# Kernel tuning notes

Hardware: AMD Instinct MI355X
Metric: run time of the kernel (lower is better)

The kernel has to match this reference:

```python
import jax, jax.numpy as jnp
import numpy as np

B, S, H, NH = 1, 2048, 1024, 16
HD = H // NH
LAYER_NUMBER = 1
EPS = 1e-5
NEG_INF = -1e9


def _layernorm(x, g, b):
    mu = jnp.mean(x, axis=-1, keepdims=True)
    var = jnp.mean((x - mu) ** 2, axis=-1, keepdims=True)
    return (x - mu) * jax.lax.rsqrt(var + EPS) * g + b


def _bloom_gelu(x):
    # tanh approximation used by Megatron/Bloom
    return x * 0.5 * (1.0 + jnp.tanh(0.79788456 * x * (1.0 + 0.044715 * x * x)))


def setup_inputs() -> dict:
    key = jax.random.key(0)
    ks = jax.random.split(key, 8)

    def w(k, shape, scale=0.02):
        return jax.random.normal(k, shape, jnp.float32) * scale

    # additive causal mask: 0 where attended, -1e9 where masked
    causal = jnp.where(jnp.tril(jnp.ones((S, S), bool)), 0.0, NEG_INF).astype(jnp.float32)
    attention_mask = causal[None, None]  # [1,1,S,S]

    return {
        "hidden_states": jax.random.normal(ks[0], (B, S, H), jnp.float32),
        "attention_mask": attention_mask,
        "alibi": w(ks[1], (B * NH, 1, S), 1.0),
        "ln1_g": jnp.ones((H,), jnp.float32),
        "ln1_b": jnp.zeros((H,), jnp.float32),
        "qkv_w": w(ks[2], (3 * H, H)),
        "qkv_b": jnp.zeros((3 * H,), jnp.float32),
        "dense_w": w(ks[3], (H, H)),
        "dense_b": jnp.zeros((H,), jnp.float32),
        "ln2_g": jnp.ones((H,), jnp.float32),
        "ln2_b": jnp.zeros((H,), jnp.float32),
        "fc1_w": w(ks[4], (4 * H, H)),
        "fc1_b": jnp.zeros((4 * H,), jnp.float32),
        "fc2_w": w(ks[5], (H, 4 * H)),
        "fc2_b": jnp.zeros((H,), jnp.float32),
    }


def reference(hidden_states, attention_mask, alibi,
              ln1_g, ln1_b, qkv_w, qkv_b, dense_w, dense_b,
              ln2_g, ln2_b, fc1_w, fc1_b, fc2_w, fc2_b):
    dtype = hidden_states.dtype
    norm_factor = np.sqrt(HD).astype(np.float32) * LAYER_NUMBER
    beta = 1.0 / LAYER_NUMBER

    # --- input layernorm (residual = pre-LN hidden states) ---
    ln_out = _layernorm(hidden_states, ln1_g, ln1_b)
    residual = hidden_states

    # --- attention ---
    fused = ln_out @ qkv_w.T + qkv_b                      # [B,S,3H]
    fused = fused.reshape(B, S, NH, 3 * HD)
    q, k, v = fused[..., :HD], fused[..., HD:2 * HD], fused[..., 2 * HD:]

    scores = jnp.einsum('bqhd,bkhd->bhqk', q, k) / norm_factor \
             + beta * alibi.reshape(B, NH, 1, S)          # [B,NH,S,S]
    attn = scores * LAYER_NUMBER + attention_mask
    attn = jnp.maximum(attn, jnp.finfo(attn.dtype).min)
    probs = jax.nn.softmax(attn.astype(jnp.float32), axis=-1).astype(dtype)
    probs = probs * (attention_mask == 0.0)               # zero out masked positions

    ctx = jnp.einsum('bhqk,bkhd->bqhd', probs, v).reshape(B, S, H)
    attn_out = ctx @ dense_w.T + dense_b + residual       # dropout_add, p=0

    # --- post-attention layernorm + MLP ---
    ln2_out = _layernorm(attn_out, ln2_g, ln2_b)
    residual2 = attn_out
    h = _bloom_gelu(ln2_out @ fc1_w.T + fc1_b)            # [B,S,4H]
    out = h @ fc2_w.T + fc2_b + residual2                 # dropout_add, p=0
    return out
```

## Files before the change

### kernel.cpp

```cpp
#include <hip/hip_runtime.h>
#include <hip/hip_bf16.h>

typedef unsigned short u16;
typedef __attribute__((ext_vector_type(8))) short bf16x8;
typedef __attribute__((ext_vector_type(4))) float f32x4;

typedef __attribute__((address_space(1))) const void cgvoid;
typedef __attribute__((address_space(3))) void lvoid;

static __device__ __forceinline__ u16 f2bf(float x) {
    __hip_bfloat16 h = __float2bfloat16(x);
    return __builtin_bit_cast(u16, h);
}

static __device__ __forceinline__ void gload_lds16(const u16* g, u16* l) {
    __builtin_amdgcn_global_load_lds((cgvoid*)g, (lvoid*)l, 16, 0, 0);
}

__global__ __launch_bounds__(256) void cvt_f32_bf16(
    const float* __restrict__ in, u16* __restrict__ out, int n4)
{
    int i = blockIdx.x * blockDim.x + threadIdx.x;
    const int stride = gridDim.x * blockDim.x;
    for (; i < n4; i += stride) {
        const float4 v = ((const float4*)in)[i];
        ushort4 pk;
        pk.x = f2bf(v.x); pk.y = f2bf(v.y); pk.z = f2bf(v.z); pk.w = f2bf(v.w);
        ((ushort4*)out)[i] = pk;
    }
}

__global__ __launch_bounds__(256) void ln_bf16(
    const float* __restrict__ x, const float* __restrict__ gw,
    const float* __restrict__ bw, u16* __restrict__ out)
{
    const int row = blockIdx.x;
    const int t = threadIdx.x;
    const float4 v = ((const float4*)(x + (size_t)row * 1024))[t];
    float s  = v.x + v.y + v.z + v.w;
    float sq = v.x*v.x + v.y*v.y + v.z*v.z + v.w*v.w;
#pragma unroll
    for (int d = 1; d < 64; d <<= 1) {
        s  += __shfl_xor(s, d, 64);
        sq += __shfl_xor(sq, d, 64);
    }
    __shared__ float ss[4], ssq[4];
    const int wave = t >> 6, lane = t & 63;
    if (lane == 0) { ss[wave] = s; ssq[wave] = sq; }
    __syncthreads();
    s  = ss[0] + ss[1] + ss[2] + ss[3];
    sq = ssq[0] + ssq[1] + ssq[2] + ssq[3];
    const float mu = s * (1.f / 1024.f);
    const float rinv = rsqrtf(sq * (1.f / 1024.f) - mu * mu + 1e-5f);
    const float4 gv = ((const float4*)gw)[t];
    const float4 bv = ((const float4*)bw)[t];
    ushort4 pk;
    pk.x = f2bf((v.x - mu) * rinv * gv.x + bv.x);
    pk.y = f2bf((v.y - mu) * rinv * gv.y + bv.y);
    pk.z = f2bf((v.z - mu) * rinv * gv.z + bv.z);
    pk.w = f2bf((v.w - mu) * rinv * gv.w + bv.w);
    ((ushort4*)(out + (size_t)row * 1024))[t] = pk;
}

template<int EPI, int BN>
__global__ __launch_bounds__(256, 4) void gemm_bt(
    const u16* __restrict__ A, const u16* __restrict__ Bw,
    const float* __restrict__ bias, void* __restrict__ Cout,
    float* __restrict__ p0, float* __restrict__ pext,
    int M, int N, int K, int Kspan)
{
    constexpr int WC = BN / 64;
    constexpr int MI = (BN == 128) ? 4 : 2;
    constexpr int NI = 4;
    __shared__ __align__(16) u16 As[128 * 64];
    __shared__ __align__(16) u16 Bs[BN * 64];
    const int t = threadIdx.x;
    const int lane = t & 63;
    const int wave = t >> 6;
    const int wr = wave / WC, wc = wave % WC;
    const int g = lane >> 4, r16 = lane & 15;
    const int tile_m = blockIdx.x * 128;
    const int tile_n = blockIdx.y * BN;
    const int kb = blockIdx.z * Kspan;

    f32x4 acc[MI][NI] = {};

    for (int k0 = kb; k0 < kb + Kspan; k0 += 64) {
        __syncthreads();
#pragma unroll
        for (int i = 0; i < 4; ++i) {
            const int off = (t + i * 256) * 8;
            const int row = off >> 6;
            const int col = off & 63;
            gload_lds16(A + (size_t)(tile_m + row) * K + k0 + col, As + off);
        }
#pragma unroll
        for (int i = 0; i < BN / 32; ++i) {
            const int off = (t + i * 256) * 8;
            const int row = off >> 6;
            const int col = off & 63;
            gload_lds16(Bw + (size_t)(tile_n + row) * K + k0 + col, Bs + off);
        }
        __syncthreads();

        bf16x8 af[MI][2], bfr[NI][2];
#pragma unroll
        for (int mi = 0; mi < MI; ++mi)
#pragma unroll
            for (int ks = 0; ks < 2; ++ks)
                af[mi][ks] = *(const bf16x8*)(As + (wr*(MI*16) + mi*16 + r16)*64 + ks*32 + g*8);
#pragma unroll
        for (int ni = 0; ni < NI; ++ni)
#pragma unroll
            for (int ks = 0; ks < 2; ++ks)
                bfr[ni][ks] = *(const bf16x8*)(Bs + (wc*64 + ni*16 + r16)*64 + ks*32 + g*8);
#pragma unroll
        for (int mi = 0; mi < MI; ++mi)
#pragma unroll
            for (int ni = 0; ni < NI; ++ni) {
                acc[mi][ni] = __builtin_amdgcn_mfma_f32_16x16x32_bf16(af[mi][0], bfr[ni][0], acc[mi][ni], 0, 0, 0);
                acc[mi][ni] = __builtin_amdgcn_mfma_f32_16x16x32_bf16(af[mi][1], bfr[ni][1], acc[mi][ni], 0, 0, 0);
            }
    }

    float* dst = nullptr;
    if constexpr (EPI == 4)
        dst = (blockIdx.z == 0) ? p0 : pext + (size_t)(blockIdx.z - 1) * ((size_t)M * N);

#pragma unroll
    for (int mi = 0; mi < MI; ++mi) {
#pragma unroll
        for (int ni = 0; ni < NI; ++ni) {
            const int col = tile_n + wc*64 + ni*16 + r16;
            const int row0 = tile_m + wr*(MI*16) + mi*16 + g*4;
#pragma unroll
            for (int r = 0; r < 4; ++r) {
                const int row = row0 + r;
                if constexpr (EPI == 4) {
                    dst[(size_t)row * N + col] = acc[mi][ni][r];
                } else if constexpr (EPI == 0) {
                    ((u16*)Cout)[(size_t)row * N + col] = f2bf(acc[mi][ni][r] + bias[col]);
                } else {
                    const float v = acc[mi][ni][r] + bias[col];
                    const float c = 0.79788456f * v * (1.0f + 0.044715f * v * v);
                    ((u16*)Cout)[(size_t)row * N + col] = f2bf(v / (1.0f + __expf(-2.0f * c)));
                }
            }
        }
    }
}

template<int NP>
__global__ __launch_bounds__(256) void reduce_bias_res(
    const float* __restrict__ p0, const float* __restrict__ pext,
    const float* __restrict__ bias, const float* __restrict__ res,
    float* __restrict__ out, int n4, int n4row)
{
    int i = blockIdx.x * blockDim.x + threadIdx.x;
    const int stride = gridDim.x * blockDim.x;
    for (; i < n4; i += stride) {
        float4 a = ((const float4*)p0)[i];
#pragma unroll
        for (int j = 0; j < NP - 1; ++j) {
            const float4 b = ((const float4*)pext)[(size_t)j * n4 + i];
            a.x += b.x; a.y += b.y; a.z += b.z; a.w += b.w;
        }
        const float4 bv = ((const float4*)bias)[i & (n4row - 1)];
        const float4 rv = ((const float4*)res)[i];
        float4 o;
        o.x = a.x + bv.x + rv.x;
        o.y = a.y + bv.y + rv.y;
        o.z = a.z + bv.z + rv.z;
        o.w = a.w + bv.w + rv.w;
        ((float4*)out)[i] = o;
    }
}

__global__ __launch_bounds__(256) void pack_kv(
    const u16* __restrict__ fused, u16* __restrict__ kP, u16* __restrict__ vP)
{
    const int bid = blockIdx.x;
    const int h = bid >> 5, kt = bid & 31;
    const int kt0 = kt * 64;
    const int t = threadIdx.x;
    const int lane = t & 63;
    const int g = lane >> 4, r16 = lane & 15;
    const size_t tbase = ((size_t)(h * 32 + kt)) * 4096;

#pragma unroll
    for (int half = 0; half < 2; ++half) {
        const int gi = (t >> 6) + half * 4;
        const int kn = gi >> 1, ks = gi & 1;
        const int w = 32*(kn>>1) + 8*(r16>>2) + 4*(kn&1) + (r16&3);
        const bf16x8 kv = *(const bf16x8*)(fused + (size_t)(kt0 + w) * 3072 + h*192 + 64 + ks*32 + g*8);
        *(bf16x8*)(kP + tbase + gi*512 + lane*8) = kv;
        union { bf16x8 v; u16 e[8]; } uv;
        const u16* vs = fused + (size_t)(kt0 + ks*32 + g*8) * 3072 + h*192 + 128 + kn*16 + r16;
#pragma unroll
        for (int e = 0; e < 8; ++e) uv.e[e] = vs[(size_t)e * 3072];
        *(bf16x8*)(vP + tbase + gi*512 + lane*8) = uv.v;
    }
}

__global__ __launch_bounds__(256, 4) void attn_swapped(
    const u16* __restrict__ fused, const u16* __restrict__ kP,
    const u16* __restrict__ vP, const float* __restrict__ alibi,
    u16* __restrict__ ctx)
{
    const int bid = blockIdx.x;
    const int h = bid & 15;
    const int qt = 127 - (bid >> 4);
    const int qw0 = qt * 16;
    const int t = threadIdx.x;
    const int lane = t & 63, wave = t >> 6;
    const int g = lane >> 4, r16 = lane & 15;
    const int qrow = qw0 + r16;

    __shared__ float Ms[4][16], Ls[4][16];
    __shared__ float Os[4][4][16][17];

    const u16* qbase = fused + (size_t)qrow * 3072 + h * 192;
    bf16x8 qf[2];
    qf[0] = *(const bf16x8*)(qbase + g*8);
    qf[1] = *(const bf16x8*)(qbase + 32 + g*8);

    f32x4 o_acc[4] = {};
    float m_r = -3.0e38f, l_r = 0.f;

    const u16* kPh = kP + (size_t)h * 32 * 4096;
    const u16* vPh = vP + (size_t)h * 32 * 4096;
    const float* abase = alibi + (size_t)h * 2048;

    const int nkt = (qw0 >> 6) + 1;
    for (int kt = wave; kt < nkt; kt += 4) {
        const int kt0 = kt * 64;
        const u16* kT = kPh + (size_t)kt * 4096;
        const u16* vT = vPh + (size_t)kt * 4096;

        bf16x8 kf[4][2], vf[4][2];
#pragma unroll
        for (int kn = 0; kn < 4; ++kn) {
            kf[kn][0] = *(const bf16x8*)(kT + (kn*2 + 0)*512 + lane*8);
            kf[kn][1] = *(const bf16x8*)(kT + (kn*2 + 1)*512 + lane*8);
        }
        float4 al[4];
#pragma unroll
        for (int kn = 0; kn < 4; ++kn)
            al[kn] = *(const float4*)(abase + kt0 + 32*(kn>>1) + 8*g + 4*(kn&1));
#pragma unroll
        for (int nd = 0; nd < 4; ++nd) {
            vf[nd][0] = *(const bf16x8*)(vT + (nd*2 + 0)*512 + lane*8);
            vf[nd][1] = *(const bf16x8*)(vT + (nd*2 + 1)*512 + lane*8);
        }

        f32x4 sc[4] = {};
#pragma unroll
        for (int kn = 0; kn < 4; ++kn) {
            sc[kn] = __builtin_amdgcn_mfma_f32_16x16x32_bf16(kf[kn][0], qf[0], sc[kn], 0, 0, 0);
            sc[kn] = __builtin_amdgcn_mfma_f32_16x16x32_bf16(kf[kn][1], qf[1], sc[kn], 0, 0, 0);
        }

        float s[4][4];
        float rmax = -3.0e38f;
#pragma unroll
        for (int kn = 0; kn < 4; ++kn) {
            const int kb = kt0 + 32*(kn>>1) + 8*g + 4*(kn&1);
            const float alv[4] = {al[kn].x, al[kn].y, al[kn].z, al[kn].w};
#pragma unroll
            for (int r = 0; r < 4; ++r) {
                float v = sc[kn][r] * 0.125f + alv[r];
                v = (kb + r <= qrow) ? v : -1.0e30f;
                s[kn][r] = v;
                rmax = fmaxf(rmax, v);
            }
        }
        rmax = fmaxf(rmax, __shfl_xor(rmax, 16, 64));
        rmax = fmaxf(rmax, __shfl_xor(rmax, 32, 64));

        const float mnew = fmaxf(m_r, rmax);
        const float scale = __expf(m_r - mnew);
        m_r = mnew;

        float psum = 0.f;
        u16 ph[4][4];
#pragma unroll
        for (int kn = 0; kn < 4; ++kn)
#pragma unroll
            for (int r = 0; r < 4; ++r) {
                const float p = __expf(s[kn][r] - mnew);
                psum += p;
                ph[kn][r] = f2bf(p);
            }
        psum += __shfl_xor(psum, 16, 64);
        psum += __shfl_xor(psum, 32, 64);
        l_r = l_r * scale + psum;

#pragma unroll
        for (int nd = 0; nd < 4; ++nd)
#pragma unroll
            for (int r = 0; r < 4; ++r)
                o_acc[nd][r] *= scale;

        bf16x8 pf[2];
#pragma unroll
        for (int ks = 0; ks < 2; ++ks) {
            union { bf16x8 v; u16 e[8]; } u;
#pragma unroll
            for (int r = 0; r < 4; ++r) { u.e[r] = ph[2*ks][r]; u.e[4+r] = ph[2*ks+1][r]; }
            pf[ks] = u.v;
        }
#pragma unroll
        for (int nd = 0; nd < 4; ++nd) {
            o_acc[nd] = __builtin_amdgcn_mfma_f32_16x16x32_bf16(vf[nd][0], pf[0], o_acc[nd], 0, 0, 0);
            o_acc[nd] = __builtin_amdgcn_mfma_f32_16x16x32_bf16(vf[nd][1], pf[1], o_acc[nd], 0, 0, 0);
        }
    }

#pragma unroll
    for (int nd = 0; nd < 4; ++nd)
#pragma unroll
        for (int r = 0; r < 4; ++r)
            Os[wave][nd][g*4 + r][r16] = o_acc[nd][r];
    if (g == 0) { Ms[wave][r16] = m_r; Ls[wave][r16] = l_r; }
    __syncthreads();

    if (wave == 0) {
        const float m0 = Ms[0][r16], m1 = Ms[1][r16], m2 = Ms[2][r16], m3 = Ms[3][r16];
        const float ms = fmaxf(fmaxf(m0, m1), fmaxf(m2, m3));
        const float f0 = __expf(m0 - ms), f1 = __expf(m1 - ms);
        const float f2 = __expf(m2 - ms), f3 = __expf(m3 - ms);
        const float l = f0*Ls[0][r16] + f1*Ls[1][r16] + f2*Ls[2][r16] + f3*Ls[3][r16];
        const float inv = 1.0f / l;
#pragma unroll
        for (int nd = 0; nd < 4; ++nd) {
            float v[4];
#pragma unroll
            for (int r = 0; r < 4; ++r) {
                const int d = g*4 + r;
                v[r] = (f0*Os[0][nd][d][r16] + f1*Os[1][nd][d][r16] +
                        f2*Os[2][nd][d][r16] + f3*Os[3][nd][d][r16]) * inv;
            }
            ushort4 pk;
            pk.x = f2bf(v[0]); pk.y = f2bf(v[1]); pk.z = f2bf(v[2]); pk.w = f2bf(v[3]);
            *(ushort4*)(ctx + (size_t)qrow * 1024 + h*64 + nd*16 + g*4) = pk;
        }
    }
}

extern "C" void kernel_launch(void* const* d_in, const int* in_sizes, int n_in,
                              void* d_out, int out_size, void* d_ws, size_t ws_size,
                              hipStream_t stream)
{
    (void)in_sizes; (void)n_in; (void)out_size; (void)ws_size;
    const float* hidden  = (const float*)d_in[0];
    const float* alibi   = (const float*)d_in[2];
    const float* ln1_g   = (const float*)d_in[3];
    const float* ln1_b   = (const float*)d_in[4];
    const float* qkv_w   = (const float*)d_in[5];
    const float* qkv_b   = (const float*)d_in[6];
    const float* dense_w = (const float*)d_in[7];
    const float* dense_b = (const float*)d_in[8];
    const float* ln2_g   = (const float*)d_in[9];
    const float* ln2_b   = (const float*)d_in[10];
    const float* fc1_w   = (const float*)d_in[11];
    const float* fc1_b   = (const float*)d_in[12];
    const float* fc2_w   = (const float*)d_in[13];
    const float* fc2_b   = (const float*)d_in[14];
    float* out = (float*)d_out;

    char* p = (char*)d_ws;
    u16* ln_buf   = (u16*)p;  p += (size_t)2048 * 1024 * 2;
    u16* qkv_wb   = (u16*)p;  p += (size_t)3072 * 1024 * 2;
    u16* fusedq   = (u16*)p;  p += (size_t)2048 * 3072 * 2;
    u16* ctx      = (u16*)p;  p += (size_t)2048 * 1024 * 2;
    u16* dense_wb = (u16*)p;  p += (size_t)1024 * 1024 * 2;
    float* attn_o = (float*)p; p += (size_t)2048 * 1024 * 4;
    u16* fc1_wb   = (u16*)p;  p += (size_t)4096 * 1024 * 2;
    u16* fc2_wb   = (u16*)p;  p += (size_t)1024 * 4096 * 2;
    float* pext   = (float*)p; p += (size_t)3 * 2048 * 1024 * 4;
    u16* hbuf = fusedq;
    u16* kP = (u16*)attn_o;
    u16* vP = kP + (size_t)16 * 32 * 4096;
    float* part0 = (float*)d_ws;

    cvt_f32_bf16<<<2048, 256, 0, stream>>>(qkv_w,   qkv_wb,   3072*1024/4);
    cvt_f32_bf16<<<1024, 256, 0, stream>>>(dense_w, dense_wb, 1024*1024/4);
    cvt_f32_bf16<<<2048, 256, 0, stream>>>(fc1_w,   fc1_wb,   4096*1024/4);
    cvt_f32_bf16<<<2048, 256, 0, stream>>>(fc2_w,   fc2_wb,   1024*4096/4);

    ln_bf16<<<2048, 256, 0, stream>>>(hidden, ln1_g, ln1_b, ln_buf);
    gemm_bt<0,64><<<dim3(16, 48), 256, 0, stream>>>(ln_buf, qkv_wb, qkv_b, fusedq,
                                                    nullptr, nullptr, 2048, 3072, 1024, 1024);
    pack_kv<<<512, 256, 0, stream>>>(fusedq, kP, vP);
    attn_swapped<<<2048, 256, 0, stream>>>(fusedq, kP, vP, alibi, ctx);
    gemm_bt<4,64><<<dim3(16, 16, 2), 256, 0, stream>>>(ctx, dense_wb, nullptr, nullptr,
                                                       part0, pext, 2048, 1024, 1024, 512);
    reduce_bias_res<2><<<2048, 256, 0, stream>>>(part0, pext, dense_b, hidden, attn_o,
                                                 2048*1024/4, 256);
    ln_bf16<<<2048, 256, 0, stream>>>(attn_o, ln2_g, ln2_b, ln_buf);
    gemm_bt<2,64><<<dim3(16, 64), 256, 0, stream>>>(ln_buf, fc1_wb, fc1_b, hbuf,
                                                    nullptr, nullptr, 2048, 4096, 1024, 1024);
    gemm_bt<4,64><<<dim3(16, 16, 4), 256, 0, stream>>>(hbuf, fc2_wb, nullptr, nullptr,
                                                       part0, pext, 2048, 1024, 4096, 1024);
    reduce_bias_res<4><<<2048, 256, 0, stream>>>(part0, pext, fc2_b, attn_o, out,
                                                 2048*1024/4, 256);
}
```

Baseline: 177.7 us.

## Fuse weight conversions with LN1 and split-K reduce with LN2

```diff
diff --git a/kernel.cpp b/kernel.cpp
--- a/kernel.cpp
+++ b/kernel.cpp
@@ -17,49 +17,60 @@
     __builtin_amdgcn_global_load_lds((cgvoid*)g, (lvoid*)l, 16, 0, 0);
 }
 
-__global__ __launch_bounds__(256) void cvt_f32_bf16(
-    const float* __restrict__ in, u16* __restrict__ out, int n4)
-{
-    int i = blockIdx.x * blockDim.x + threadIdx.x;
-    const int stride = gridDim.x * blockDim.x;
-    for (; i < n4; i += stride) {
-        const float4 v = ((const float4*)in)[i];
+__global__ __launch_bounds__(256) void prep(
+    const float* __restrict__ hidden, const float* __restrict__ g1,
+    const float* __restrict__ b1, u16* __restrict__ ln_out,
+    const float* __restrict__ qkv_w, const float* __restrict__ dense_w,
+    const float* __restrict__ fc1_w, const float* __restrict__ fc2_w,
+    u16* __restrict__ qkv_wb, u16* __restrict__ dense_wb,
+    u16* __restrict__ fc1_wb, u16* __restrict__ fc2_wb)
+{
+    const int t = threadIdx.x;
+    if (blockIdx.x < 2048) {
+        const int row = blockIdx.x;
+        const float4 v = ((const float4*)(hidden + (size_t)row * 1024))[t];
+        float s  = v.x + v.y + v.z + v.w;
+        float sq = v.x*v.x + v.y*v.y + v.z*v.z + v.w*v.w;
+#pragma unroll
+        for (int d = 1; d < 64; d <<= 1) {
+            s  += __shfl_xor(s, d, 64);
+            sq += __shfl_xor(sq, d, 64);
+        }
+        __shared__ float ss[4], ssq[4];
+        const int wave = t >> 6, lane = t & 63;
+        if (lane == 0) { ss[wave] = s; ssq[wave] = sq; }
+        __syncthreads();
+        s  = ss[0] + ss[1] + ss[2] + ss[3];
+        sq = ssq[0] + ssq[1] + ssq[2] + ssq[3];
+        const float mu = s * (1.f / 1024.f);
+        const float rinv = rsqrtf(sq * (1.f / 1024.f) - mu * mu + 1e-5f);
+        const float4 gv = ((const float4*)g1)[t];
+        const float4 bv = ((const float4*)b1)[t];
+        ushort4 pk;
+        pk.x = f2bf((v.x - mu) * rinv * gv.x + bv.x);
+        pk.y = f2bf((v.y - mu) * rinv * gv.y + bv.y);
+        pk.z = f2bf((v.z - mu) * rinv * gv.z + bv.z);
+        pk.w = f2bf((v.w - mu) * rinv * gv.w + bv.w);
+        ((ushort4*)(ln_out + (size_t)row * 1024))[t] = pk;
+        return;
+    }
+    constexpr int C0 = 786432;
+    constexpr int C1 = C0 + 262144;
+    constexpr int C2 = C1 + 1048576;
+    constexpr int C3 = C2 + 1048576;
+    int i = (blockIdx.x - 2048) * 256 + t;
+    const int stride = (gridDim.x - 2048) * 256;
+    for (; i < C3; i += stride) {
+        const float* src; u16* dst; int j;
+        if (i < C0)      { src = qkv_w;   dst = qkv_wb;   j = i; }
+        else if (i < C1) { src = dense_w; dst = dense_wb; j = i - C0; }
+        else if (i < C2) { src = fc1_w;   dst = fc1_wb;   j = i - C1; }
+        else             { src = fc2_w;   dst = fc2_wb;   j = i - C2; }
+        const float4 v = ((const float4*)src)[j];
         ushort4 pk;
         pk.x = f2bf(v.x); pk.y = f2bf(v.y); pk.z = f2bf(v.z); pk.w = f2bf(v.w);
-        ((ushort4*)out)[i] = pk;
-    }
-}
-
-__global__ __launch_bounds__(256) void ln_bf16(
-    const float* __restrict__ x, const float* __restrict__ gw,
-    const float* __restrict__ bw, u16* __restrict__ out)
-{
-    const int row = blockIdx.x;
-    const int t = threadIdx.x;
-    const float4 v = ((const float4*)(x + (size_t)row * 1024))[t];
-    float s  = v.x + v.y + v.z + v.w;
-    float sq = v.x*v.x + v.y*v.y + v.z*v.z + v.w*v.w;
-#pragma unroll
-    for (int d = 1; d < 64; d <<= 1) {
-        s  += __shfl_xor(s, d, 64);
-        sq += __shfl_xor(sq, d, 64);
-    }
-    __shared__ float ss[4], ssq[4];
-    const int wave = t >> 6, lane = t & 63;
-    if (lane == 0) { ss[wave] = s; ssq[wave] = sq; }
-    __syncthreads();
-    s  = ss[0] + ss[1] + ss[2] + ss[3];
-    sq = ssq[0] + ssq[1] + ssq[2] + ssq[3];
-    const float mu = s * (1.f / 1024.f);
-    const float rinv = rsqrtf(sq * (1.f / 1024.f) - mu * mu + 1e-5f);
-    const float4 gv = ((const float4*)gw)[t];
-    const float4 bv = ((const float4*)bw)[t];
-    ushort4 pk;
-    pk.x = f2bf((v.x - mu) * rinv * gv.x + bv.x);
-    pk.y = f2bf((v.y - mu) * rinv * gv.y + bv.y);
-    pk.z = f2bf((v.z - mu) * rinv * gv.z + bv.z);
-    pk.w = f2bf((v.w - mu) * rinv * gv.w + bv.w);
-    ((ushort4*)(out + (size_t)row * 1024))[t] = pk;
+        ((ushort4*)dst)[j] = pk;
+    }
 }
 
 template<int EPI, int BN>
@@ -148,6 +159,51 @@
             }
         }
     }
+}
+
+__global__ __launch_bounds__(256) void reduce2_ln(
+    const float* __restrict__ p0, const float* __restrict__ p1,
+    const float* __restrict__ bias, const float* __restrict__ res,
+    float* __restrict__ attn_o, const float* __restrict__ g2,
+    const float* __restrict__ b2, u16* __restrict__ ln_out)
+{
+    const int row = blockIdx.x;
+    const int t = threadIdx.x;
+    const size_t i = (size_t)row * 256 + t;
+    const float4 a0 = ((const float4*)p0)[i];
+    const float4 a1 = ((const float4*)p1)[i];
+    const float4 bv = ((const float4*)bias)[t];
+    const float4 rv = ((const float4*)res)[i];
+    float4 v;
+    v.x = a0.x + a1.x + bv.x + rv.x;
+    v.y = a0.y + a1.y + bv.y + rv.y;
+    v.z = a0.z + a1.z + bv.z + rv.z;
+    v.w = a0.w + a1.w + bv.w + rv.w;
+    ((float4*)attn_o)[i] = v;
+
+    float s  = v.x + v.y + v.z + v.w;
+    float sq = v.x*v.x + v.y*v.y + v.z*v.z + v.w*v.w;
+#pragma unroll
+    for (int d = 1; d < 64; d <<= 1) {
+        s  += __shfl_xor(s, d, 64);
+        sq += __shfl_xor(sq, d, 64);
+    }
+    __shared__ float ss[4], ssq[4];
+    const int wave = t >> 6, lane = t & 63;
+    if (lane == 0) { ss[wave] = s; ssq[wave] = sq; }
+    __syncthreads();
+    s  = ss[0] + ss[1] + ss[2] + ss[3];
+    sq = ssq[0] + ssq[1] + ssq[2] + ssq[3];
+    const float mu = s * (1.f / 1024.f);
+    const float rinv = rsqrtf(sq * (1.f / 1024.f) - mu * mu + 1e-5f);
+    const float4 gv = ((const float4*)g2)[t];
+    const float4 b2v = ((const float4*)b2)[t];
+    ushort4 pk;
+    pk.x = f2bf((v.x - mu) * rinv * gv.x + b2v.x);
+    pk.y = f2bf((v.y - mu) * rinv * gv.y + b2v.y);
+    pk.z = f2bf((v.z - mu) * rinv * gv.z + b2v.z);
+    pk.w = f2bf((v.w - mu) * rinv * gv.w + b2v.w);
+    ((ushort4*)(ln_out + (size_t)row * 1024))[t] = pk;
 }
 
 template<int NP>
@@ -378,26 +434,22 @@
     u16* fc1_wb   = (u16*)p;  p += (size_t)4096 * 1024 * 2;
     u16* fc2_wb   = (u16*)p;  p += (size_t)1024 * 4096 * 2;
     float* pext   = (float*)p; p += (size_t)3 * 2048 * 1024 * 4;
+    float* part0  = (float*)p; p += (size_t)2048 * 1024 * 4;
     u16* hbuf = fusedq;
     u16* kP = (u16*)attn_o;
     u16* vP = kP + (size_t)16 * 32 * 4096;
-    float* part0 = (float*)d_ws;
-
-    cvt_f32_bf16<<<2048, 256, 0, stream>>>(qkv_w,   qkv_wb,   3072*1024/4);
-    cvt_f32_bf16<<<1024, 256, 0, stream>>>(dense_w, dense_wb, 1024*1024/4);
-    cvt_f32_bf16<<<2048, 256, 0, stream>>>(fc1_w,   fc1_wb,   4096*1024/4);
-    cvt_f32_bf16<<<2048, 256, 0, stream>>>(fc2_w,   fc2_wb,   1024*4096/4);
-
-    ln_bf16<<<2048, 256, 0, stream>>>(hidden, ln1_g, ln1_b, ln_buf);
+
+    prep<<<6144, 256, 0, stream>>>(hidden, ln1_g, ln1_b, ln_buf,
+                                   qkv_w, dense_w, fc1_w, fc2_w,
+                                   qkv_wb, dense_wb, fc1_wb, fc2_wb);
     gemm_bt<0,64><<<dim3(16, 48), 256, 0, stream>>>(ln_buf, qkv_wb, qkv_b, fusedq,
                                                     nullptr, nullptr, 2048, 3072, 1024, 1024);
     pack_kv<<<512, 256, 0, stream>>>(fusedq, kP, vP);
     attn_swapped<<<2048, 256, 0, stream>>>(fusedq, kP, vP, alibi, ctx);
     gemm_bt<4,64><<<dim3(16, 16, 2), 256, 0, stream>>>(ctx, dense_wb, nullptr, nullptr,
                                                        part0, pext, 2048, 1024, 1024, 512);
-    reduce_bias_res<2><<<2048, 256, 0, stream>>>(part0, pext, dense_b, hidden, attn_o,
-                                                 2048*1024/4, 256);
-    ln_bf16<<<2048, 256, 0, stream>>>(attn_o, ln2_g, ln2_b, ln_buf);
+    reduce2_ln<<<2048, 256, 0, stream>>>(part0, pext, dense_b, hidden, attn_o,
+                                         ln2_g, ln2_b, ln_buf);
     gemm_bt<2,64><<<dim3(16, 64), 256, 0, stream>>>(ln_buf, fc1_wb, fc1_b, hbuf,
                                                     nullptr, nullptr, 2048, 4096, 1024, 1024);
     gemm_bt<4,64><<<dim3(16, 16, 4), 256, 0, stream>>>(hbuf, fc2_wb, nullptr, nullptr,
```

After: 166.8 us. 1.07x faster.
